# Kernel tuning notes

Hardware: AMD Instinct MI355X
Metric: run time of the kernel (lower is better)

Reference implementation:

```python
import jax, jax.numpy as jnp
import numpy as np

NEG = -10000.0
EMB = 64
HID = 128


def _lstm_dir(x_tbf, Wih, Whh, b):
    # x_tbf: [T, B, EMB]; Wih: [4H, EMB]; Whh: [4H, H]; b: [4H]
    B = x_tbf.shape[1]
    h0 = jnp.zeros((B, HID), x_tbf.dtype)
    c0 = jnp.zeros((B, HID), x_tbf.dtype)

    def step(carry, xt):
        h, c = carry
        z = xt @ Wih.T + h @ Whh.T + b  # [B, 4H]
        i, f, g, o = jnp.split(z, 4, axis=-1)
        c = jax.nn.sigmoid(f) * c + jax.nn.sigmoid(i) * jnp.tanh(g)
        h = jax.nn.sigmoid(o) * jnp.tanh(c)
        return (h, c), h

    _, hs = jax.lax.scan(step, (h0, c0), x_tbf)
    return hs  # [T, B, H]


def _crf_logZ(feats, trans):
    # feats: [B, T, K]; trans[next, prev]
    B, T, K = feats.shape
    fv0 = jnp.full((B, K), NEG, feats.dtype).at[:, 0].set(0.0)

    def step(fv, emit_t):  # fv [B,K], emit_t [B,K]
        s = fv[:, None, :] + trans[None, :, :] + emit_t[:, :, None]  # [B,next,prev]
        return jax.nn.logsumexp(s, axis=2), None

    fv, _ = jax.lax.scan(step, fv0, jnp.swapaxes(feats, 0, 1))
    return jax.nn.logsumexp(fv + trans[0][None, :], axis=1)  # [B]


def _gold_score(feats, tags, trans):
    # feats: [B,T,K], tags: [B,T]
    B, T, K = feats.shape
    prev = jnp.concatenate([jnp.zeros((B, 1), tags.dtype), tags[:, :-1]], axis=1)
    trans_sc = trans[tags, prev].sum(axis=1)  # [B]
    emit_sc = jnp.take_along_axis(feats, tags[:, :, None], axis=2)[..., 0].sum(axis=1)
    stop_sc = trans[0, tags[:, -1]]
    return trans_sc + emit_sc + stop_sc


def setup_inputs() -> dict:
    key = jax.random.key(0)
    ks = jax.random.split(key, 12)
    V, K, B, T = 32000, 32, 128, 512
    sentences = jax.random.randint(ks[0], (B, T), 0, V)
    tags = jax.random.randint(ks[1], (B, T), 0, K)
    emb = jax.random.normal(ks[2], (V, EMB), jnp.float32) * 0.1
    s_ih = 1.0 / np.sqrt(HID)
    Wih_f = jax.random.uniform(ks[3], (4 * HID, EMB), jnp.float32, -s_ih, s_ih)
    Whh_f = jax.random.uniform(ks[4], (4 * HID, HID), jnp.float32, -s_ih, s_ih)
    b_f = jax.random.uniform(ks[5], (4 * HID,), jnp.float32, -s_ih, s_ih)
    Wih_b = jax.random.uniform(ks[6], (4 * HID, EMB), jnp.float32, -s_ih, s_ih)
    Whh_b = jax.random.uniform(ks[7], (4 * HID, HID), jnp.float32, -s_ih, s_ih)
    b_b = jax.random.uniform(ks[8], (4 * HID,), jnp.float32, -s_ih, s_ih)
    s_o = 1.0 / np.sqrt(2 * HID)
    W_out = jax.random.uniform(ks[9], (K, 2 * HID), jnp.float32, -s_o, s_o)
    b_out = jax.random.uniform(ks[10], (K,), jnp.float32, -s_o, s_o)
    trans = jax.random.normal(ks[11], (K, K), jnp.float32)
    trans = trans.at[:, 0].set(NEG).at[0, :].set(NEG)
    return {"sentences": sentences, "tags": tags, "emb": emb,
            "Wih_f": Wih_f, "Whh_f": Whh_f, "b_f": b_f,
            "Wih_b": Wih_b, "Whh_b": Whh_b, "b_b": b_b,
            "W_out": W_out, "b_out": b_out, "trans": trans}


def reference(sentences, tags, emb, Wih_f, Whh_f, b_f, Wih_b, Whh_b, b_b, W_out, b_out, trans):
    x = emb[sentences]                      # [B, T, EMB]
    x_tbf = jnp.swapaxes(x, 0, 1)           # [T, B, EMB]
    h_f = _lstm_dir(x_tbf, Wih_f, Whh_f, b_f)
    h_b = _lstm_dir(x_tbf[::-1], Wih_b, Whh_b, b_b)[::-1]
    h = jnp.concatenate([h_f, h_b], axis=-1)  # [T, B, 256]
    feats = jnp.swapaxes(h, 0, 1) @ W_out.T + b_out  # [B, T, K]
    logZ = _crf_logZ(feats, trans)
    gold = _gold_score(feats, tags, trans)
    return logZ.sum() - gold.sum()
```

## Files before the change

kernel.cpp:

```cpp
#include <hip/hip_runtime.h>
#include <stdint.h>

typedef short bf16x8 __attribute__((ext_vector_type(8)));
typedef float f32x4 __attribute__((ext_vector_type(4)));

#define NEG (-10000.0f)
#define LOG2E 1.44269504089f
#define LN2 0.69314718056f
#define EXP2F(x) __builtin_amdgcn_exp2f(x)
#define LOG2F(x) __builtin_amdgcn_logf(x)
#define RCPF(x) __builtin_amdgcn_rcpf(x)
constexpr int T_LEN = 512;
constexpr int BATCH = 128;

__device__ __forceinline__ unsigned short f2bf(float f) {
    union { float f; unsigned u; } v; v.f = f;
    return (unsigned short)((v.u + 0x7FFFu + ((v.u >> 16) & 1u)) >> 16);
}
__device__ __forceinline__ float bf2f(unsigned short s) {
    union { unsigned u; float f; } v; v.u = (unsigned)s << 16; return v.f;
}
__device__ __forceinline__ unsigned short f2bf_fast(float f) {
    unsigned r;
    asm("v_cvt_pk_bf16_f32 %0, %1, %2" : "=v"(r) : "v"(f), "v"(f));
    return (unsigned short)r;
}
__device__ __forceinline__ f32x4 mfma16(bf16x8 a, bf16x8 b, f32x4 c) {
    return __builtin_amdgcn_mfma_f32_16x16x32_bf16(a, b, c, 0, 0, 0);
}

__global__ void __launch_bounds__(256) k_embed(const int* __restrict__ sent,
                                               const float* __restrict__ emb,
                                               unsigned short* __restrict__ xt) {
    int gid = blockIdx.x * 256 + threadIdx.x;
    int row = gid >> 5;
    int p   = gid & 31;
    int w = sent[row];
    float2 v = *(const float2*)(emb + (size_t)w * 64 + p * 2);
    unsigned o;
    asm("v_cvt_pk_bf16_f32 %0, %1, %2" : "=v"(o) : "v"(v.x), "v"(v.y));
    ((unsigned*)xt)[(size_t)row * 32 + p] = o;
}

__global__ void __launch_bounds__(512, 2) k_lstm(
        const unsigned short* __restrict__ xt,
        const float* __restrict__ Wih_f, const float* __restrict__ Whh_f, const float* __restrict__ b_f,
        const float* __restrict__ Wih_b, const float* __restrict__ Whh_b, const float* __restrict__ b_b,
        unsigned short* __restrict__ hbuf) {
    const int tid  = threadIdx.x;
    const int lane = tid & 63;
    const int w    = tid >> 6;
    const int b    = blockIdx.x & 127;
    const int dir  = blockIdx.x >> 7;

    const float* Wih  = dir ? Wih_b : Wih_f;
    const float* Whh  = dir ? Whh_b : Whh_f;
    const float* bias = dir ? b_b   : b_f;

    __shared__ __align__(16) unsigned short zbuf[2][32][512];
    __shared__ __align__(16) unsigned short hl[2][128];

    const int nlo = lane & 15;
    const int kg  = lane >> 4;
    const int u   = 16 * w + nlo;

    bf16x8 hfrag[4][4];
    #pragma unroll
    for (int g = 0; g < 4; ++g) {
        const float sc = (g == 2) ? (-2.0f * LOG2E) : (-LOG2E);
        const int j = 128 * g + u;
        #pragma unroll
        for (int kt = 0; kt < 4; ++kt) {
            const float* src = Whh + (size_t)j * 128 + 32 * kt + kg * 8;
            bf16x8 tmp;
            #pragma unroll
            for (int q = 0; q < 8; ++q) tmp[q] = (short)f2bf(src[q] * sc);
            hfrag[g][kt] = tmp;
        }
    }
    bf16x8 wx[4][2];
    float bsc[4];
    #pragma unroll
    for (int nt = 0; nt < 4; ++nt) {
        const int n = 64 * w + 16 * nt + nlo;
        const float scn = ((n >> 7) == 2) ? (-2.0f * LOG2E) : (-LOG2E);
        bsc[nt] = bias[n] * scn;
        #pragma unroll
        for (int kt = 0; kt < 2; ++kt) {
            const float* src = Wih + (size_t)n * 64 + 32 * kt + kg * 8;
            bf16x8 tmp;
            #pragma unroll
            for (int q = 0; q < 8; ++q) tmp[q] = (short)f2bf(src[q] * scn);
            wx[nt][kt] = tmp;
        }
    }

    const unsigned short* xb = xt + (size_t)b * T_LEN * 64;

    auto load_x = [&](int c, bf16x8 xf[2][2]) {
        const int tb = dir ? (511 - 32 * c) : (32 * c);
        #pragma unroll
        for (int rt = 0; rt < 2; ++rt) {
            const int m = 16 * rt + nlo;
            const int t = dir ? (tb - m) : (tb + m);
            xf[rt][0] = *(const bf16x8*)(xb + t * 64 + kg * 8);
            xf[rt][1] = *(const bf16x8*)(xb + t * 64 + 32 + kg * 8);
        }
    };
    auto zx_phase = [&](int buf, bf16x8 xf[2][2]) {
        #pragma unroll
        for (int rt = 0; rt < 2; ++rt) {
            #pragma unroll
            for (int nt = 0; nt < 4; ++nt) {
                f32x4 a = (f32x4){bsc[nt], bsc[nt], bsc[nt], bsc[nt]};
                a = mfma16(xf[rt][0], wx[nt][0], a);
                a = mfma16(xf[rt][1], wx[nt][1], a);
                const int n = 64 * w + 16 * nt + nlo;
                const int base = (n & 127) * 4 + (n >> 7);
                #pragma unroll
                for (int r = 0; r < 4; ++r)
                    zbuf[buf][16 * rt + 4 * kg + r][base] = f2bf(a[r]);
            }
        }
    };

    if (tid < 128) { hl[0][tid] = 0; hl[1][tid] = 0; }
    bf16x8 xfA[2][2], xfB[2][2];
    load_x(0, xfA);
    zx_phase(0, xfA);
    load_x(1, xfB);
    __syncthreads();

    float c = 0.0f;
    const f32x4 z4 = (f32x4){0.f, 0.f, 0.f, 0.f};
    unsigned short* hb = hbuf + ((size_t)b * T_LEN) * 256 + dir * 128 + u;

    for (int ch = 0; ch < 16; ++ch) {
        const int p = ch & 1;
        if (ch + 1 < 16) zx_phase(1 - p, p ? xfA : xfB);
        if (ch + 2 < 16) load_x(ch + 2, p ? xfB : xfA);

        for (int s = 0; s < 32; ++s) {
            const int gs = 32 * ch + s;
            const int hp = gs & 1;

            ushort4 zv = *(const ushort4*)(&zbuf[p][s][u * 4]);
            const unsigned short* hr = hl[hp];
            bf16x8 h0 = *(const bf16x8*)(hr      + kg * 8);
            bf16x8 h1 = *(const bf16x8*)(hr + 32 + kg * 8);
            bf16x8 h2 = *(const bf16x8*)(hr + 64 + kg * 8);
            bf16x8 h3 = *(const bf16x8*)(hr + 96 + kg * 8);

            f32x4 ai = mfma16(h0, hfrag[0][0], z4);
            f32x4 af = mfma16(h0, hfrag[1][0], z4);
            f32x4 ag = mfma16(h0, hfrag[2][0], z4);
            f32x4 ao = mfma16(h0, hfrag[3][0], z4);
            #pragma unroll
            for (int kt = 1; kt < 4; ++kt) {
                bf16x8 hh = (kt == 1) ? h1 : (kt == 2) ? h2 : h3;
                ai = mfma16(hh, hfrag[0][kt], ai);
                af = mfma16(hh, hfrag[1][kt], af);
                ag = mfma16(hh, hfrag[2][kt], ag);
                ao = mfma16(hh, hfrag[3][kt], ao);
            }

            float zi = bf2f(zv.x), zf = bf2f(zv.y), zg = bf2f(zv.z), zo = bf2f(zv.w);
            float ig = RCPF(1.0f + EXP2F(ai[0] + zi));
            float fg = RCPF(1.0f + EXP2F(af[0] + zf));
            float tg = 2.0f * RCPF(1.0f + EXP2F(ag[0] + zg)) - 1.0f;
            float og = RCPF(1.0f + EXP2F(ao[0] + zo));
            c = fg * c + ig * tg;
            float tc = 2.0f * RCPF(1.0f + EXP2F(-2.0f * LOG2E * c)) - 1.0f;
            unsigned short hv = f2bf_fast(og * tc);

            if (kg == 0) {
                hl[1 - hp][u] = hv;
                const int t_src = dir ? (511 - gs) : gs;
                hb[(size_t)t_src * 256] = hv;
            }
            __asm__ volatile("" ::: "memory");
            __builtin_amdgcn_s_waitcnt(0xc07f);
            __builtin_amdgcn_s_barrier();
            __asm__ volatile("" ::: "memory");
        }
    }
}

__global__ void __launch_bounds__(256) k_feats(const unsigned short* __restrict__ hbuf,
                                               const float* __restrict__ Wout,
                                               const float* __restrict__ bout,
                                               float* __restrict__ feats) {
    const int lane = threadIdx.x & 63;
    const int wv   = blockIdx.x * 4 + (threadIdx.x >> 6);
    const int nlo  = lane & 15, kg = lane >> 4;

    bf16x8 bw[2][8];
    #pragma unroll
    for (int nt = 0; nt < 2; ++nt) {
        const float* src0 = Wout + (size_t)(nt * 16 + nlo) * 256 + kg * 8;
        #pragma unroll
        for (int kt = 0; kt < 8; ++kt) {
            bf16x8 tmp;
            #pragma unroll
            for (int q = 0; q < 8; ++q) tmp[q] = (short)f2bf(src0[kt * 32 + q]);
            bw[nt][kt] = tmp;
        }
    }
    float bb0 = bout[nlo], bb1 = bout[16 + nlo];

    for (int rg = 0; rg < 4; ++rg) {
        int row0 = wv * 64 + rg * 16;
        f32x4 a0 = {0.f,0.f,0.f,0.f}, a1 = {0.f,0.f,0.f,0.f};
        #pragma unroll
        for (int kt = 0; kt < 8; ++kt) {
            bf16x8 a = *(const bf16x8*)(hbuf + (size_t)(row0 + nlo) * 256 + kt * 32 + kg * 8);
            a0 = mfma16(a, bw[0][kt], a0);
            a1 = mfma16(a, bw[1][kt], a1);
        }
        #pragma unroll
        for (int r = 0; r < 4; ++r) {
            size_t rr = (size_t)(row0 + kg * 4 + r) * 32;
            feats[rr + nlo]      = a0[r] + bb0;
            feats[rr + 16 + nlo] = a1[r] + bb1;
        }
    }
}

__global__ void __launch_bounds__(64) k_crf(const float* __restrict__ feats,
                                            const float* __restrict__ trans,
                                            const int* __restrict__ tags,
                                            float* __restrict__ out) {
    const int b    = blockIdx.x;
    const int lane = threadIdx.x;
    const int k1   = lane & 31;
    const int half = lane >> 5;

    __shared__ float str[1024];
    for (int i = lane; i < 1024; i += 64) str[i] = trans[i];

    float tr2[16];
    #pragma unroll
    for (int j = 0; j < 16; ++j) tr2[j] = trans[k1 * 32 + half * 16 + j] * LOG2E;
    float E[16];
    #pragma unroll
    for (int j = 0; j < 16; ++j) E[j] = EXP2F(tr2[j]);
    __syncthreads();

    const int* tg = tags + (size_t)b * T_LEN;
    const float* fb = feats + (size_t)b * T_LEN * 32;
    float gsum = 0.0f;
    for (int t = lane; t < T_LEN; t += 64) {
        int cur = tg[t];
        int prev = t ? tg[t - 1] : 0;
        gsum += str[cur * 32 + prev] + fb[(size_t)t * 32 + cur];
    }
    #pragma unroll
    for (int o = 32; o >= 1; o >>= 1) gsum += __shfl_xor(gsum, o);

    float fv2  = (k1 == 0) ? 0.0f : NEG * LOG2E;
    float coff = NEG * LOG2E;
    float ev2  = fb[k1] * LOG2E;

    {
        float evn = fb[32 + k1];
        float p0 = 0.f, p1 = 0.f, p2 = 0.f, p3 = 0.f;
        #pragma unroll
        for (int j = 0; j < 16; j += 4) {
            float f0 = __shfl(fv2, half * 16 + j);
            float f1 = __shfl(fv2, half * 16 + j + 1);
            float f2 = __shfl(fv2, half * 16 + j + 2);
            float f3 = __shfl(fv2, half * 16 + j + 3);
            p0 += EXP2F(f0 + tr2[j]     - coff);
            p1 += EXP2F(f1 + tr2[j + 1] - coff);
            p2 += EXP2F(f2 + tr2[j + 2] - coff);
            p3 += EXP2F(f3 + tr2[j + 3] - coff);
        }
        float p = (p0 + p1) + (p2 + p3);
        p += __shfl_xor(p, 32);
        p = fmaxf(p, 1e-37f);
        fv2  = coff + LOG2F(p) + ev2;
        coff = __shfl(fv2, 16);
        ev2  = evn * LOG2E;
    }

    for (int t = 1; t < T_LEN; ++t) {
        float evn = (t + 1 < T_LEN) ? fb[(size_t)(t + 1) * 32 + k1] : 0.0f;
        float u = EXP2F(fv2 - coff);
        float p0 = 0.f, p1 = 0.f, p2 = 0.f, p3 = 0.f;
        #pragma unroll
        for (int j = 0; j < 16; j += 4) {
            float u0 = __shfl(u, half * 16 + j);
            float u1 = __shfl(u, half * 16 + j + 1);
            float u2 = __shfl(u, half * 16 + j + 2);
            float u3 = __shfl(u, half * 16 + j + 3);
            p0 += E[j]     * u0;
            p1 += E[j + 1] * u1;
            p2 += E[j + 2] * u2;
            p3 += E[j + 3] * u3;
        }
        float p = (p0 + p1) + (p2 + p3);
        p += __shfl_xor(p, 32);
        p = fmaxf(p, 1e-37f);
        fv2  = coff + LOG2F(p) + ev2;
        coff = __shfl(fv2, 16);
        ev2  = evn * LOG2E;
    }

    float v2 = fv2 + str[k1] * LOG2E;
    float m2 = v2;
    #pragma unroll
    for (int o = 32; o >= 1; o >>= 1) m2 = fmaxf(m2, __shfl_xor(m2, o));
    float e = EXP2F(v2 - m2);
    #pragma unroll
    for (int o = 32; o >= 1; o >>= 1) e += __shfl_xor(e, o);
    float logZ = LN2 * (m2 + LOG2F(e) - 1.0f);

    if (lane == 0) {
        float gold = gsum + str[tg[T_LEN - 1]];
        atomicAdd(out, logZ - gold);
    }
}

extern "C" void kernel_launch(void* const* d_in, const int* in_sizes, int n_in,
                              void* d_out, int out_size, void* d_ws, size_t ws_size,
                              hipStream_t stream) {
    const int*   sent  = (const int*)d_in[0];
    const int*   tags  = (const int*)d_in[1];
    const float* emb   = (const float*)d_in[2];
    const float* Wih_f = (const float*)d_in[3];
    const float* Whh_f = (const float*)d_in[4];
    const float* b_f   = (const float*)d_in[5];
    const float* Wih_b = (const float*)d_in[6];
    const float* Whh_b = (const float*)d_in[7];
    const float* b_b   = (const float*)d_in[8];
    const float* Wout  = (const float*)d_in[9];
    const float* bout  = (const float*)d_in[10];
    const float* trans = (const float*)d_in[11];
    (void)in_sizes; (void)n_in; (void)ws_size;

    char* ws = (char*)d_ws;
    unsigned short* hbuf  = (unsigned short*)ws;
    float*          feats = (float*)(ws + 33554432);
    unsigned short* xt    = (unsigned short*)(ws + 33554432 + 8388608);

    (void)hipMemsetAsync(d_out, 0, sizeof(float) * out_size, stream);
    k_embed<<<8192, 256, 0, stream>>>(sent, emb, xt);
    k_lstm <<<256,  512, 0, stream>>>(xt, Wih_f, Whh_f, b_f, Wih_b, Whh_b, b_b, hbuf);
    k_feats<<<256,  256, 0, stream>>>(hbuf, Wout, bout, feats);
    k_crf  <<<BATCH, 64, 0, stream>>>(feats, trans, tags, (float*)d_out);
}
```

Before: 450.8 us.

## Break MFMA accumulation chains in LSTM step and simplify CRF forward loop

The LSTM recurrence step now issues sixteen independent MFMAs, one per gate and k-tile, and sums the partial results in registers. This replaces four dependent accumulation chains and aims to cut MFMA dependency latency on the serial critical path, at the cost of more accumulator registers and extra adds. The CRF kernel now has each lane cover all 32 previous tags, which removes the cross-half shuffle-reduce. Its first step is computed in closed form from the row sum of exp(trans), relying on the initial forward vector being zero for tag 0 and NEG elsewhere.

```diff
diff --git a/kernel.cpp b/kernel.cpp
--- a/kernel.cpp
+++ b/kernel.cpp
@@ -151,24 +151,32 @@
             bf16x8 h2 = *(const bf16x8*)(hr + 64 + kg * 8);
             bf16x8 h3 = *(const bf16x8*)(hr + 96 + kg * 8);
 
-            f32x4 ai = mfma16(h0, hfrag[0][0], z4);
-            f32x4 af = mfma16(h0, hfrag[1][0], z4);
-            f32x4 ag = mfma16(h0, hfrag[2][0], z4);
-            f32x4 ao = mfma16(h0, hfrag[3][0], z4);
-            #pragma unroll
-            for (int kt = 1; kt < 4; ++kt) {
-                bf16x8 hh = (kt == 1) ? h1 : (kt == 2) ? h2 : h3;
-                ai = mfma16(hh, hfrag[0][kt], ai);
-                af = mfma16(hh, hfrag[1][kt], af);
-                ag = mfma16(hh, hfrag[2][kt], ag);
-                ao = mfma16(hh, hfrag[3][kt], ao);
-            }
-
-            float zi = bf2f(zv.x), zf = bf2f(zv.y), zg = bf2f(zv.z), zo = bf2f(zv.w);
-            float ig = RCPF(1.0f + EXP2F(ai[0] + zi));
-            float fg = RCPF(1.0f + EXP2F(af[0] + zf));
-            float tg = 2.0f * RCPF(1.0f + EXP2F(ag[0] + zg)) - 1.0f;
-            float og = RCPF(1.0f + EXP2F(ao[0] + zo));
+            f32x4 ai0 = mfma16(h0, hfrag[0][0], z4);
+            f32x4 af0 = mfma16(h0, hfrag[1][0], z4);
+            f32x4 ag0 = mfma16(h0, hfrag[2][0], z4);
+            f32x4 ao0 = mfma16(h0, hfrag[3][0], z4);
+            f32x4 ai1 = mfma16(h1, hfrag[0][1], z4);
+            f32x4 af1 = mfma16(h1, hfrag[1][1], z4);
+            f32x4 ag1 = mfma16(h1, hfrag[2][1], z4);
+            f32x4 ao1 = mfma16(h1, hfrag[3][1], z4);
+            f32x4 ai2 = mfma16(h2, hfrag[0][2], z4);
+            f32x4 af2 = mfma16(h2, hfrag[1][2], z4);
+            f32x4 ag2 = mfma16(h2, hfrag[2][2], z4);
+            f32x4 ao2 = mfma16(h2, hfrag[3][2], z4);
+            f32x4 ai3 = mfma16(h3, hfrag[0][3], z4);
+            f32x4 af3 = mfma16(h3, hfrag[1][3], z4);
+            f32x4 ag3 = mfma16(h3, hfrag[2][3], z4);
+            f32x4 ao3 = mfma16(h3, hfrag[3][3], z4);
+
+            float zi = bf2f(zv.x) + ((ai0[0] + ai1[0]) + (ai2[0] + ai3[0]));
+            float zf = bf2f(zv.y) + ((af0[0] + af1[0]) + (af2[0] + af3[0]));
+            float zg = bf2f(zv.z) + ((ag0[0] + ag1[0]) + (ag2[0] + ag3[0]));
+            float zo = bf2f(zv.w) + ((ao0[0] + ao1[0]) + (ao2[0] + ao3[0]));
+
+            float ig = RCPF(1.0f + EXP2F(zi));
+            float fg = RCPF(1.0f + EXP2F(zf));
+            float tg = 2.0f * RCPF(1.0f + EXP2F(zg)) - 1.0f;
+            float og = RCPF(1.0f + EXP2F(zo));
             c = fg * c + ig * tg;
             float tc = 2.0f * RCPF(1.0f + EXP2F(-2.0f * LOG2E * c)) - 1.0f;
             unsigned short hv = f2bf_fast(og * tc);
@@ -233,17 +241,17 @@
     const int b    = blockIdx.x;
     const int lane = threadIdx.x;
     const int k1   = lane & 31;
-    const int half = lane >> 5;
 
     __shared__ float str[1024];
     for (int i = lane; i < 1024; i += 64) str[i] = trans[i];
 
-    float tr2[16];
-    #pragma unroll
-    for (int j = 0; j < 16; ++j) tr2[j] = trans[k1 * 32 + half * 16 + j] * LOG2E;
-    float E[16];
-    #pragma unroll
-    for (int j = 0; j < 16; ++j) E[j] = EXP2F(tr2[j]);
+    float E[32];
+    float sumE = 0.0f;
+    #pragma unroll
+    for (int j = 0; j < 32; ++j) {
+        E[j] = EXP2F(trans[k1 * 32 + j] * LOG2E);
+        sumE += E[j];
+    }
     __syncthreads();
 
     const int* tg = tags + (size_t)b * T_LEN;
@@ -257,49 +265,23 @@
     #pragma unroll
     for (int o = 32; o >= 1; o >>= 1) gsum += __shfl_xor(gsum, o);
 
-    float fv2  = (k1 == 0) ? 0.0f : NEG * LOG2E;
     float coff = NEG * LOG2E;
-    float ev2  = fb[k1] * LOG2E;
-
-    {
-        float evn = fb[32 + k1];
-        float p0 = 0.f, p1 = 0.f, p2 = 0.f, p3 = 0.f;
-        #pragma unroll
-        for (int j = 0; j < 16; j += 4) {
-            float f0 = __shfl(fv2, half * 16 + j);
-            float f1 = __shfl(fv2, half * 16 + j + 1);
-            float f2 = __shfl(fv2, half * 16 + j + 2);
-            float f3 = __shfl(fv2, half * 16 + j + 3);
-            p0 += EXP2F(f0 + tr2[j]     - coff);
-            p1 += EXP2F(f1 + tr2[j + 1] - coff);
-            p2 += EXP2F(f2 + tr2[j + 2] - coff);
-            p3 += EXP2F(f3 + tr2[j + 3] - coff);
-        }
-        float p = (p0 + p1) + (p2 + p3);
-        p += __shfl_xor(p, 32);
-        p = fmaxf(p, 1e-37f);
-        fv2  = coff + LOG2F(p) + ev2;
-        coff = __shfl(fv2, 16);
-        ev2  = evn * LOG2E;
-    }
+    float fv2  = coff + LOG2F(1.0f + sumE) + fb[k1] * LOG2E;
+    coff = __shfl(fv2, 16);
+    float ev2 = fb[32 + k1] * LOG2E;
 
     for (int t = 1; t < T_LEN; ++t) {
         float evn = (t + 1 < T_LEN) ? fb[(size_t)(t + 1) * 32 + k1] : 0.0f;
         float u = EXP2F(fv2 - coff);
         float p0 = 0.f, p1 = 0.f, p2 = 0.f, p3 = 0.f;
         #pragma unroll
-        for (int j = 0; j < 16; j += 4) {
-            float u0 = __shfl(u, half * 16 + j);
-            float u1 = __shfl(u, half * 16 + j + 1);
-            float u2 = __shfl(u, half * 16 + j + 2);
-            float u3 = __shfl(u, half * 16 + j + 3);
-            p0 += E[j]     * u0;
-            p1 += E[j + 1] * u1;
-            p2 += E[j + 2] * u2;
-            p3 += E[j + 3] * u3;
+        for (int j = 0; j < 32; j += 4) {
+            p0 += E[j]     * __shfl(u, j);
+            p1 += E[j + 1] * __shfl(u, j + 1);
+            p2 += E[j + 2] * __shfl(u, j + 2);
+            p3 += E[j + 3] * __shfl(u, j + 3);
         }
         float p = (p0 + p1) + (p2 + p3);
-        p += __shfl_xor(p, 32);
         p = fmaxf(p, 1e-37f);
         fv2  = coff + LOG2F(p) + ev2;
         coff = __shfl(fv2, 16);
```

Result: slower. 539.2 us (+19.6%).

## Use readlane broadcasts in CRF recursion and simplify LSTM h-store indexing

Applied to the files above, without the earlier changes.

The CRF forward recursion no longer splits the 32 previous-tag terms across two wave halves with ds_bpermute shuffles. Each lane now holds all 32 exp(trans) values and pulls u from lanes 0..31 with v_readlane (scalar broadcast), which removes the cross-half xor shuffle. The first timestep is computed in closed form from the sum of exp(trans), and emission loads are prefetched two steps ahead. The LSTM loop switches to a pointer-increment h store and is unrolled by 2, trading more registers for shorter dependency chains.

```diff
diff --git a/kernel.cpp b/kernel.cpp
--- a/kernel.cpp
+++ b/kernel.cpp
@@ -24,6 +24,12 @@
     unsigned r;
     asm("v_cvt_pk_bf16_f32 %0, %1, %2" : "=v"(r) : "v"(f), "v"(f));
     return (unsigned short)r;
+}
+__device__ __forceinline__ float rlanef(float x, int l) {
+    union { float f; int i; } a, r;
+    a.f = x;
+    r.i = __builtin_amdgcn_readlane(a.i, l);
+    return r.f;
 }
 __device__ __forceinline__ f32x4 mfma16(bf16x8 a, bf16x8 b, f32x4 c) {
     return __builtin_amdgcn_mfma_f32_16x16x32_bf16(a, b, c, 0, 0, 0);
@@ -133,13 +139,15 @@
 
     float c = 0.0f;
     const f32x4 z4 = (f32x4){0.f, 0.f, 0.f, 0.f};
-    unsigned short* hb = hbuf + ((size_t)b * T_LEN) * 256 + dir * 128 + u;
+    unsigned short* hbp = hbuf + ((size_t)b * T_LEN + (dir ? 511 : 0)) * 256 + dir * 128 + u;
+    const ptrdiff_t hstep = dir ? -256 : 256;
 
     for (int ch = 0; ch < 16; ++ch) {
         const int p = ch & 1;
         if (ch + 1 < 16) zx_phase(1 - p, p ? xfA : xfB);
         if (ch + 2 < 16) load_x(ch + 2, p ? xfB : xfA);
 
+        #pragma unroll 2
         for (int s = 0; s < 32; ++s) {
             const int gs = 32 * ch + s;
             const int hp = gs & 1;
@@ -175,9 +183,9 @@
 
             if (kg == 0) {
                 hl[1 - hp][u] = hv;
-                const int t_src = dir ? (511 - gs) : gs;
-                hb[(size_t)t_src * 256] = hv;
+                *hbp = hv;
             }
+            hbp += hstep;
             __asm__ volatile("" ::: "memory");
             __builtin_amdgcn_s_waitcnt(0xc07f);
             __builtin_amdgcn_s_barrier();
@@ -233,17 +241,17 @@
     const int b    = blockIdx.x;
     const int lane = threadIdx.x;
     const int k1   = lane & 31;
-    const int half = lane >> 5;
 
     __shared__ float str[1024];
     for (int i = lane; i < 1024; i += 64) str[i] = trans[i];
 
-    float tr2[16];
-    #pragma unroll
-    for (int j = 0; j < 16; ++j) tr2[j] = trans[k1 * 32 + half * 16 + j] * LOG2E;
-    float E[16];
-    #pragma unroll
-    for (int j = 0; j < 16; ++j) E[j] = EXP2F(tr2[j]);
+    float E[32];
+    float sumE = 0.0f;
+    #pragma unroll
+    for (int j = 0; j < 32; ++j) {
+        E[j] = EXP2F(trans[k1 * 32 + j] * LOG2E);
+        sumE += E[j];
+    }
     __syncthreads();
 
     const int* tg = tags + (size_t)b * T_LEN;
@@ -257,53 +265,28 @@
     #pragma unroll
     for (int o = 32; o >= 1; o >>= 1) gsum += __shfl_xor(gsum, o);
 
-    float fv2  = (k1 == 0) ? 0.0f : NEG * LOG2E;
     float coff = NEG * LOG2E;
-    float ev2  = fb[k1] * LOG2E;
-
-    {
-        float evn = fb[32 + k1];
-        float p0 = 0.f, p1 = 0.f, p2 = 0.f, p3 = 0.f;
-        #pragma unroll
-        for (int j = 0; j < 16; j += 4) {
-            float f0 = __shfl(fv2, half * 16 + j);
-            float f1 = __shfl(fv2, half * 16 + j + 1);
-            float f2 = __shfl(fv2, half * 16 + j + 2);
-            float f3 = __shfl(fv2, half * 16 + j + 3);
-            p0 += EXP2F(f0 + tr2[j]     - coff);
-            p1 += EXP2F(f1 + tr2[j + 1] - coff);
-            p2 += EXP2F(f2 + tr2[j + 2] - coff);
-            p3 += EXP2F(f3 + tr2[j + 3] - coff);
-        }
-        float p = (p0 + p1) + (p2 + p3);
-        p += __shfl_xor(p, 32);
-        p = fmaxf(p, 1e-37f);
-        fv2  = coff + LOG2F(p) + ev2;
-        coff = __shfl(fv2, 16);
-        ev2  = evn * LOG2E;
-    }
+    float fv2  = coff + LOG2F(1.0f + sumE) + fb[k1] * LOG2E;
+    coff = rlanef(fv2, 16);
+    float evA = fb[32 + k1] * LOG2E;
+    float evB = fb[64 + k1] * LOG2E;
 
     for (int t = 1; t < T_LEN; ++t) {
-        float evn = (t + 1 < T_LEN) ? fb[(size_t)(t + 1) * 32 + k1] : 0.0f;
+        float evC = (t + 2 < T_LEN) ? fb[(size_t)(t + 2) * 32 + k1] : 0.0f;
         float u = EXP2F(fv2 - coff);
         float p0 = 0.f, p1 = 0.f, p2 = 0.f, p3 = 0.f;
         #pragma unroll
-        for (int j = 0; j < 16; j += 4) {
-            float u0 = __shfl(u, half * 16 + j);
-            float u1 = __shfl(u, half * 16 + j + 1);
-            float u2 = __shfl(u, half * 16 + j + 2);
-            float u3 = __shfl(u, half * 16 + j + 3);
-            p0 += E[j]     * u0;
-            p1 += E[j + 1] * u1;
-            p2 += E[j + 2] * u2;
-            p3 += E[j + 3] * u3;
+        for (int j = 0; j < 32; j += 4) {
+            p0 += E[j]     * rlanef(u, j);
+            p1 += E[j + 1] * rlanef(u, j + 1);
+            p2 += E[j + 2] * rlanef(u, j + 2);
+            p3 += E[j + 3] * rlanef(u, j + 3);
         }
         float p = (p0 + p1) + (p2 + p3);
-        p += __shfl_xor(p, 32);
         p = fmaxf(p, 1e-37f);
-        fv2  = coff + LOG2F(p) + ev2;
-        coff = __shfl(fv2, 16);
-        ev2  = evn * LOG2E;
+        fv2  = coff + LOG2F(p) + evA;
+        coff = rlanef(fv2, 16);
+        evA = evB; evB = evC * LOG2E;
     }
 
     float v2 = fv2 + str[k1] * LOG2E;
```

Result: faster. 440.0 us (-2.4%).
